# Performance work log

Measured on AMD Instinct MI355X. Metric: run time of the kernel, lower is better.

## Reference

```python
import jax, jax.numpy as jnp
import numpy as np

N_NODES = 50000


def _sage_mean(x, src, dst, Wl, bl, Wr, n_nodes):
    # PyG SAGEConv (aggr='mean', root_weight=True): lin_l(mean_j x_j) + lin_r(x_i)
    msgs = x[src]                                             # [E, F] gather
    agg = jax.ops.segment_sum(msgs, dst, num_segments=n_nodes)  # [N, F]
    cnt = jax.ops.segment_sum(jnp.ones((src.shape[0],), x.dtype), dst,
                              num_segments=n_nodes)           # [N]
    mean = agg / jnp.maximum(cnt, 1.0)[:, None]
    return mean @ Wl + bl + x @ Wr


def setup_inputs() -> dict:
    key = jax.random.key(0)
    ks = jax.random.split(key, 12)
    in_ft = 64
    o0, o1, o2 = 64, 128, 128
    d2 = o0 + o0          # conv2 in = 128
    d3 = o0 + o0 + o1     # conv3 in = 256
    E = 800000

    def lin(k, fi, fo):
        s = 1.0 / np.sqrt(fi)
        return jax.random.uniform(k, (fi, fo), jnp.float32, -s, s)

    x = jax.random.normal(ks[0], (N_NODES, in_ft), jnp.float32)
    edge_index = jax.random.randint(ks[1], (2, E), 0, N_NODES, jnp.int64)
    return {
        "x": x,
        "edge_index": edge_index,
        "Wp": lin(ks[2], in_ft, o0), "bp": jnp.zeros((o0,), jnp.float32),
        "Wl1": lin(ks[3], in_ft, o0), "bl1": jnp.zeros((o0,), jnp.float32),
        "Wr1": lin(ks[4], in_ft, o0),
        "Wl2": lin(ks[5], d2, o1), "bl2": jnp.zeros((o1,), jnp.float32),
        "Wr2": lin(ks[6], d2, o1),
        "Wl3": lin(ks[7], d3, o2), "bl3": jnp.zeros((o2,), jnp.float32),
        "Wr3": lin(ks[8], d3, o2),
    }


def reference(x, edge_index, Wp, bp, Wl1, bl1, Wr1, Wl2, bl2, Wr2, Wl3, bl3, Wr3):
    src, dst = edge_index[0], edge_index[1]
    act = jax.nn.relu
    x_p = act(x @ Wp + bp)                                        # [N, o0]
    h1 = act(_sage_mean(x, src, dst, Wl1, bl1, Wr1, N_NODES))      # [N, o0]
    in2 = jnp.concatenate([x_p, h1], axis=1)                      # [N, 2*o0]
    h2 = act(_sage_mean(in2, src, dst, Wl2, bl2, Wr2, N_NODES))    # [N, o1]
    in3 = jnp.concatenate([x_p, h1, h2], axis=1)                  # [N, 2*o0+o1]
    h3 = act(_sage_mean(in3, src, dst, Wl3, bl3, Wr3, N_NODES))    # [N, o2]
    return h3
```

## Files before the change

### kernel.cpp

```cpp
#include <hip/hip_runtime.h>

#define N_NODES 50000
#define ELLW 48

typedef unsigned int uint;
typedef unsigned short ushort;
typedef float floatx4 __attribute__((ext_vector_type(4)));
typedef short short8 __attribute__((ext_vector_type(8)));

__device__ inline ushort f2bf(float f) {
    uint u = __float_as_uint(f);
    return (ushort)((u + 0x7fffu + ((u >> 16) & 1u)) >> 16);
}
__device__ inline float bflo(uint u) { return __uint_as_float(u << 16); }
__device__ inline float bfhi(uint u) { return __uint_as_float(u & 0xffff0000u); }


__device__ inline void swz_body(const float* __restrict__ W, ushort* __restrict__ Wz,
                                int O, int t) {
    int lane = t & 63, cb = t >> 6;
    int NBm = O / 16;
    int c = cb / NBm, nb = cb % NBm;
    int quad = lane >> 4, l16 = lane & 15;
#pragma unroll
    for (int j = 0; j < 8; j++) {
        float v = W[(size_t)(c * 32 + quad * 8 + j) * O + nb * 16 + l16];
        Wz[(size_t)t * 8 + j] = f2bf(v);
    }
}

__device__ void gemm1_body(int gb, const float* __restrict__ x,
                           const float* __restrict__ Wp, const float* __restrict__ bp,
                           ushort* __restrict__ feats, ushort* ldsA) {
    constexpr int LDA = 40;
    const int tid = threadIdx.x;
    const int wave = tid >> 6, lane = tid & 63;
    const int quad = lane >> 4, l16 = lane & 15;
    const int node0 = gb * 64;

    floatx4 acc[4];
#pragma unroll
    for (int nb = 0; nb < 4; nb++) acc[nb] = (floatx4){0.f, 0.f, 0.f, 0.f};

#pragma unroll
    for (int kk = 0; kk < 2; kk++) {
        const int k0 = kk * 32;
        __syncthreads();
        {
            int row = tid >> 2, seg = tid & 3;
            int node = node0 + row;
            float4 v0 = {0.f,0.f,0.f,0.f}, v1 = {0.f,0.f,0.f,0.f};
            if (node < N_NODES) {
                v0 = *(const float4*)&x[(size_t)node * 64 + k0 + seg * 8];
                v1 = *(const float4*)&x[(size_t)node * 64 + k0 + seg * 8 + 4];
            }
            ushort4 o0, o1;
            o0.x = f2bf(v0.x); o0.y = f2bf(v0.y); o0.z = f2bf(v0.z); o0.w = f2bf(v0.w);
            o1.x = f2bf(v1.x); o1.y = f2bf(v1.y); o1.z = f2bf(v1.z); o1.w = f2bf(v1.w);
            *(ushort4*)&ldsA[row * LDA + seg * 8] = o0;
            *(ushort4*)&ldsA[row * LDA + seg * 8 + 4] = o1;
        }
        __syncthreads();

        short8 a = *(const short8*)&ldsA[(wave * 16 + l16) * LDA + quad * 8];
#pragma unroll
        for (int nb = 0; nb < 4; nb++) {
            short8 bfrag;
#pragma unroll
            for (int j = 0; j < 8; j++)
                bfrag[j] = (short)f2bf(Wp[(size_t)(k0 + quad * 8 + j) * 64 + nb * 16 + l16]);
            acc[nb] = __builtin_amdgcn_mfma_f32_16x16x32_bf16(a, bfrag, acc[nb], 0, 0, 0);
        }
    }

#pragma unroll
    for (int nb = 0; nb < 4; nb++) {
        int ncol = nb * 16 + l16;
        float bv = bp[ncol];
#pragma unroll
        for (int r = 0; r < 4; r++) {
            int node = node0 + wave * 16 + quad * 4 + r;
            if (node >= N_NODES) continue;
            float v = fmaxf(acc[nb][r] + bv, 0.f);
            feats[(size_t)node * 256 + ncol] = f2bf(v);
        }
    }
}

__global__ __launch_bounds__(256) void k1_mega(
    const int* __restrict__ src, const int* __restrict__ dst, int E,
    int* __restrict__ fillc, ushort* __restrict__ ell,
    const float* __restrict__ x, ushort* __restrict__ xb,
    const float* __restrict__ Wp, const float* __restrict__ bp, ushort* __restrict__ feats,
    const float* __restrict__ Wl1, ushort* __restrict__ zl1,
    const float* __restrict__ Wr1, ushort* __restrict__ zr1,
    const float* __restrict__ Wl2, ushort* __restrict__ zl2,
    const float* __restrict__ Wr2, ushort* __restrict__ zr2,
    const float* __restrict__ Wl3, ushort* __restrict__ zl3,
    const float* __restrict__ Wr3, ushort* __restrict__ zr3,
    int NF, int NG, int NC)
{
    __shared__ ushort ldsA[64 * 40];
    int b = blockIdx.x, tid = threadIdx.x;
    if (b < NF) {
        int t = b * 256 + tid;
        if (t < E) {
            int d = dst[t], s = src[t];
            int p = atomicAdd(&fillc[d], 1);
            if (p < ELLW) ell[(size_t)d * ELLW + p] = (ushort)s;
        }
        return;
    }
    b -= NF;
    if (b < NG) { gemm1_body(b, x, Wp, bp, feats, ldsA); return; }
    b -= NG;
    if (b < NC) {
        int t = b * 256 + tid;
        float4 v = ((const float4*)x)[t];
        ushort4 o;
        o.x = f2bf(v.x); o.y = f2bf(v.y); o.z = f2bf(v.z); o.w = f2bf(v.w);
        ((ushort4*)xb)[t] = o;
        return;
    }
    b -= NC;
    if      (b < 2)  swz_body(Wl1, zl1, 64,  (b - 0) * 256 + tid);
    else if (b < 4)  swz_body(Wr1, zr1, 64,  (b - 2) * 256 + tid);
    else if (b < 12) swz_body(Wl2, zl2, 128, (b - 4) * 256 + tid);
    else if (b < 20) swz_body(Wr2, zr2, 128, (b - 12) * 256 + tid);
    else if (b < 36) swz_body(Wl3, zl3, 128, (b - 20) * 256 + tid);
    else             swz_body(Wr3, zr3, 128, (b - 36) * 256 + tid);
}


__global__ __launch_bounds__(256) void gather64_k(const int* __restrict__ fillc,
                                                  const ushort* __restrict__ ell,
                                                  const ushort* __restrict__ in, int sin,
                                                  ushort* __restrict__ out, int sout) {
    int node = blockIdx.x * 4 + (threadIdx.x >> 6);
    if (node >= N_NODES) return;
    int lane = threadIdx.x & 63;
    int sub = lane >> 3, c = lane & 7;
    int n = fillc[node]; int nc = (n > ELLW) ? ELLW : n;
    const ushort* base = ell + (size_t)node * ELLW;
    float a[8];
#pragma unroll
    for (int j = 0; j < 8; j++) a[j] = 0.f;

    int i = sub;
    for (; i + 8 < nc; i += 16) {
        uint4 u0 = *(const uint4*)&in[(size_t)base[i] * sin + 8 * c];
        uint4 u1 = *(const uint4*)&in[(size_t)base[i + 8] * sin + 8 * c];
        a[0] += bflo(u0.x) + bflo(u1.x);  a[1] += bfhi(u0.x) + bfhi(u1.x);
        a[2] += bflo(u0.y) + bflo(u1.y);  a[3] += bfhi(u0.y) + bfhi(u1.y);
        a[4] += bflo(u0.z) + bflo(u1.z);  a[5] += bfhi(u0.z) + bfhi(u1.z);
        a[6] += bflo(u0.w) + bflo(u1.w);  a[7] += bfhi(u0.w) + bfhi(u1.w);
    }
    if (i < nc) {
        uint4 u0 = *(const uint4*)&in[(size_t)base[i] * sin + 8 * c];
        a[0] += bflo(u0.x);  a[1] += bfhi(u0.x);
        a[2] += bflo(u0.y);  a[3] += bfhi(u0.y);
        a[4] += bflo(u0.z);  a[5] += bfhi(u0.z);
        a[6] += bflo(u0.w);  a[7] += bfhi(u0.w);
    }
#pragma unroll
    for (int d = 8; d < 64; d <<= 1)
#pragma unroll
        for (int j = 0; j < 8; j++) a[j] += __shfl_xor(a[j], d);
    if (sub == 0) {
        float iv = 1.0f / fmaxf((float)n, 1.0f);
        uint4 r;
        r.x = (uint)f2bf(a[0] * iv) | ((uint)f2bf(a[1] * iv) << 16);
        r.y = (uint)f2bf(a[2] * iv) | ((uint)f2bf(a[3] * iv) << 16);
        r.z = (uint)f2bf(a[4] * iv) | ((uint)f2bf(a[5] * iv) << 16);
        r.w = (uint)f2bf(a[6] * iv) | ((uint)f2bf(a[7] * iv) << 16);
        *(uint4*)&out[(size_t)node * sout + 8 * c] = r;
    }
}

__global__ __launch_bounds__(256) void gather128_k(const int* __restrict__ fillc,
                                                   const ushort* __restrict__ ell,
                                                   const ushort* __restrict__ in, int sin,
                                                   ushort* __restrict__ out, int sout) {
    int node = blockIdx.x * 4 + (threadIdx.x >> 6);
    if (node >= N_NODES) return;
    int lane = threadIdx.x & 63;
    int sub = lane >> 4, c = lane & 15;
    int n = fillc[node]; int nc = (n > ELLW) ? ELLW : n;
    const ushort* base = ell + (size_t)node * ELLW;
    float a[8];
#pragma unroll
    for (int j = 0; j < 8; j++) a[j] = 0.f;

    int i = sub;
    for (; i + 12 < nc; i += 16) {
        uint4 u0 = *(const uint4*)&in[(size_t)base[i] * sin + 8 * c];
        uint4 u1 = *(const uint4*)&in[(size_t)base[i + 4] * sin + 8 * c];
        uint4 u2 = *(const uint4*)&in[(size_t)base[i + 8] * sin + 8 * c];
        uint4 u3 = *(const uint4*)&in[(size_t)base[i + 12] * sin + 8 * c];
        a[0] += (bflo(u0.x) + bflo(u1.x)) + (bflo(u2.x) + bflo(u3.x));
        a[1] += (bfhi(u0.x) + bfhi(u1.x)) + (bfhi(u2.x) + bfhi(u3.x));
        a[2] += (bflo(u0.y) + bflo(u1.y)) + (bflo(u2.y) + bflo(u3.y));
        a[3] += (bfhi(u0.y) + bfhi(u1.y)) + (bfhi(u2.y) + bfhi(u3.y));
        a[4] += (bflo(u0.z) + bflo(u1.z)) + (bflo(u2.z) + bflo(u3.z));
        a[5] += (bfhi(u0.z) + bfhi(u1.z)) + (bfhi(u2.z) + bfhi(u3.z));
        a[6] += (bflo(u0.w) + bflo(u1.w)) + (bflo(u2.w) + bflo(u3.w));
        a[7] += (bfhi(u0.w) + bfhi(u1.w)) + (bfhi(u2.w) + bfhi(u3.w));
    }
    for (; i < nc; i += 4) {
        uint4 u0 = *(const uint4*)&in[(size_t)base[i] * sin + 8 * c];
        a[0] += bflo(u0.x);  a[1] += bfhi(u0.x);
        a[2] += bflo(u0.y);  a[3] += bfhi(u0.y);
        a[4] += bflo(u0.z);  a[5] += bfhi(u0.z);
        a[6] += bflo(u0.w);  a[7] += bfhi(u0.w);
    }
#pragma unroll
    for (int d = 16; d < 64; d <<= 1)
#pragma unroll
        for (int j = 0; j < 8; j++) a[j] += __shfl_xor(a[j], d);
    if (sub == 0) {
        float iv = 1.0f / fmaxf((float)n, 1.0f);
        uint4 r;
        r.x = (uint)f2bf(a[0] * iv) | ((uint)f2bf(a[1] * iv) << 16);
        r.y = (uint)f2bf(a[2] * iv) | ((uint)f2bf(a[3] * iv) << 16);
        r.z = (uint)f2bf(a[4] * iv) | ((uint)f2bf(a[5] * iv) << 16);
        r.w = (uint)f2bf(a[6] * iv) | ((uint)f2bf(a[7] * iv) << 16);
        *(uint4*)&out[(size_t)node * sout + 8 * c] = r;
    }
}


template <int O, bool OUT_BF16>
__global__ __launch_bounds__(256) void mfma_gemm_k(
    const ushort* __restrict__ A1, int s1, int K1, const ushort* __restrict__ Wz1,
    const ushort* __restrict__ A2, int s2, int K2, const ushort* __restrict__ Wz2,
    const float* __restrict__ bias, void* __restrict__ outp, int so, int ocol)
{
    constexpr int NB = O / 16;
    constexpr int LDA = 40;
    __shared__ ushort ldsA[64 * LDA];

    const int tid = threadIdx.x;
    const int wave = tid >> 6, lane = tid & 63;
    const int quad = lane >> 4, l16 = lane & 15;
    const int node0 = blockIdx.x * 64;

    floatx4 acc[NB];
#pragma unroll
    for (int nb = 0; nb < NB; nb++) acc[nb] = (floatx4){0.f, 0.f, 0.f, 0.f};

#pragma unroll 1
    for (int phase = 0; phase < 2; ++phase) {
        const ushort* A = phase ? A2 : A1;
        const ushort* Wz = phase ? Wz2 : Wz1;
        const int K = phase ? K2 : K1;
        const int sA = phase ? s2 : s1;

#pragma unroll 1
        for (int k0 = 0; k0 < K; k0 += 32) {
            __syncthreads();
            {
                int row = tid >> 2, seg = tid & 3;
                int node = node0 + row;
                uint4 v = {0u, 0u, 0u, 0u};
                if (node < N_NODES)
                    v = *(const uint4*)&A[(size_t)node * sA + k0 + seg * 8];
                *(uint4*)&ldsA[row * LDA + seg * 8] = v;
            }
            __syncthreads();

            short8 a = *(const short8*)&ldsA[(wave * 16 + l16) * LDA + quad * 8];
            const short8* bz = (const short8*)Wz + (size_t)(k0 >> 5) * NB * 64;
#pragma unroll
            for (int nb = 0; nb < NB; nb++) {
                short8 b = bz[nb * 64 + lane];
                acc[nb] = __builtin_amdgcn_mfma_f32_16x16x32_bf16(a, b, acc[nb], 0, 0, 0);
            }
        }
    }

#pragma unroll
    for (int nb = 0; nb < NB; nb++) {
        int ncol = nb * 16 + l16;
        float bv = bias[ncol];
#pragma unroll
        for (int r = 0; r < 4; r++) {
            int node = node0 + wave * 16 + quad * 4 + r;
            if (node >= N_NODES) continue;
            float v = fmaxf(acc[nb][r] + bv, 0.f);
            if (OUT_BF16)
                ((ushort*)outp)[(size_t)node * so + ocol + ncol] = f2bf(v);
            else
                ((float*)outp)[(size_t)node * so + ocol + ncol] = v;
        }
    }
}


extern "C" void kernel_launch(void* const* d_in, const int* in_sizes, int n_in,
                              void* d_out, int out_size, void* d_ws, size_t ws_size,
                              hipStream_t stream) {
    const float* x   = (const float*)d_in[0];
    const int*   ei  = (const int*)d_in[1];
    const float* Wp  = (const float*)d_in[2];
    const float* bp  = (const float*)d_in[3];
    const float* Wl1 = (const float*)d_in[4];
    const float* bl1 = (const float*)d_in[5];
    const float* Wr1 = (const float*)d_in[6];
    const float* Wl2 = (const float*)d_in[7];
    const float* bl2 = (const float*)d_in[8];
    const float* Wr2 = (const float*)d_in[9];
    const float* Wl3 = (const float*)d_in[10];
    const float* bl3 = (const float*)d_in[11];
    const float* Wr3 = (const float*)d_in[12];

    const int E = in_sizes[1] / 2;
    const int N = N_NODES;
    const int* src = ei;
    const int* dst = ei + E;

    char* p = (char*)d_ws;
    ushort* xb    = (ushort*)p;  p += (size_t)N * 64 * 2;
    ushort* feats = (ushort*)p;  p += (size_t)N * 256 * 2;
    ushort* aggx  = (ushort*)p;  p += (size_t)N * 64 * 2;
    ushort* aggf  = (ushort*)p;  p += (size_t)N * 256 * 2;
    int* fillc    = (int*)p;     p += (size_t)N * 4;
    ushort* ell   = (ushort*)p;  p += (size_t)N * ELLW * 2;
    ushort* zl1   = (ushort*)p;  p += 64 * 64 * 2;
    ushort* zr1   = (ushort*)p;  p += 64 * 64 * 2;
    ushort* zl2   = (ushort*)p;  p += 128 * 128 * 2;
    ushort* zr2   = (ushort*)p;  p += 128 * 128 * 2;
    ushort* zl3   = (ushort*)p;  p += 256 * 128 * 2;
    ushort* zr3   = (ushort*)p;  p += 256 * 128 * 2;

    hipMemsetAsync(fillc, 0, (size_t)N * sizeof(int), stream);

    const int NF = (E + 255) / 256;
    const int NG = (N + 63) / 64;
    const int NC = (N * 64 / 4) / 256;

    k1_mega<<<NF + NG + NC + 52, 256, 0, stream>>>(
        src, dst, E, fillc, ell, x, xb, Wp, bp, feats,
        Wl1, zl1, Wr1, zr1, Wl2, zl2, Wr2, zr2, Wl3, zl3, Wr3, zr3,
        NF, NG, NC);

    gather64_k<<<(N + 3) / 4, 256, 0, stream>>>(fillc, ell, xb, 64, aggx, 64);

    mfma_gemm_k<64, true><<<NG, 256, 0, stream>>>(
        aggx, 64, 64, zl1, xb, 64, 64, zr1, bl1, feats, 256, 64);

    gather128_k<<<(N + 3) / 4, 256, 0, stream>>>(fillc, ell, feats, 256, aggf, 256);

    mfma_gemm_k<128, true><<<NG, 256, 0, stream>>>(
        aggf, 256, 128, zl2, feats, 256, 128, zr2, bl2, feats, 256, 128);

    gather128_k<<<(N + 3) / 4, 256, 0, stream>>>(fillc, ell, feats + 128, 256, aggf + 128, 256);

    mfma_gemm_k<128, false><<<NG, 256, 0, stream>>>(
        aggf, 256, 256, zl3, feats, 256, 256, zr3, bl3, (float*)d_out, 128, 0);
}
```

Measured before the change: 291.4 us.

## Project layer-1 features before aggregation and fuse x_p gather with it

```diff
diff --git a/kernel.cpp b/kernel.cpp
--- a/kernel.cpp
+++ b/kernel.cpp
@@ -14,7 +14,9 @@
 }
 __device__ inline float bflo(uint u) { return __uint_as_float(u << 16); }
 __device__ inline float bfhi(uint u) { return __uint_as_float(u & 0xffff0000u); }
-
+__device__ inline uint pack2(float lo, float hi) {
+    return (uint)f2bf(lo) | ((uint)f2bf(hi) << 16);
+}
 
 __device__ inline void swz_body(const float* __restrict__ W, ushort* __restrict__ Wz,
                                 int O, int t) {
@@ -31,16 +33,22 @@
 
 __device__ void gemm1_body(int gb, const float* __restrict__ x,
                            const float* __restrict__ Wp, const float* __restrict__ bp,
-                           ushort* __restrict__ feats, ushort* ldsA) {
+                           const float* __restrict__ Wl1, const float* __restrict__ Wr1,
+                           ushort* __restrict__ feats, ushort* __restrict__ g1in,
+                           ushort* __restrict__ r1, ushort* ldsA) {
     constexpr int LDA = 40;
     const int tid = threadIdx.x;
     const int wave = tid >> 6, lane = tid & 63;
     const int quad = lane >> 4, l16 = lane & 15;
     const int node0 = gb * 64;
 
-    floatx4 acc[4];
-#pragma unroll
-    for (int nb = 0; nb < 4; nb++) acc[nb] = (floatx4){0.f, 0.f, 0.f, 0.f};
+    floatx4 aP[4], aY[4], aR[4];
+#pragma unroll
+    for (int nb = 0; nb < 4; nb++) {
+        aP[nb] = (floatx4){0, 0, 0, 0};
+        aY[nb] = (floatx4){0, 0, 0, 0};
+        aR[nb] = (floatx4){0, 0, 0, 0};
+    }
 
 #pragma unroll
     for (int kk = 0; kk < 2; kk++) {
@@ -49,7 +57,7 @@
         {
             int row = tid >> 2, seg = tid & 3;
             int node = node0 + row;
-            float4 v0 = {0.f,0.f,0.f,0.f}, v1 = {0.f,0.f,0.f,0.f};
+            float4 v0 = {0, 0, 0, 0}, v1 = {0, 0, 0, 0};
             if (node < N_NODES) {
                 v0 = *(const float4*)&x[(size_t)node * 64 + k0 + seg * 8];
                 v1 = *(const float4*)&x[(size_t)node * 64 + k0 + seg * 8 + 4];
@@ -65,11 +73,19 @@
         short8 a = *(const short8*)&ldsA[(wave * 16 + l16) * LDA + quad * 8];
 #pragma unroll
         for (int nb = 0; nb < 4; nb++) {
-            short8 bfrag;
+            short8 bw;
 #pragma unroll
             for (int j = 0; j < 8; j++)
-                bfrag[j] = (short)f2bf(Wp[(size_t)(k0 + quad * 8 + j) * 64 + nb * 16 + l16]);
-            acc[nb] = __builtin_amdgcn_mfma_f32_16x16x32_bf16(a, bfrag, acc[nb], 0, 0, 0);
+                bw[j] = (short)f2bf(Wp[(size_t)(k0 + quad * 8 + j) * 64 + nb * 16 + l16]);
+            aP[nb] = __builtin_amdgcn_mfma_f32_16x16x32_bf16(a, bw, aP[nb], 0, 0, 0);
+#pragma unroll
+            for (int j = 0; j < 8; j++)
+                bw[j] = (short)f2bf(Wl1[(size_t)(k0 + quad * 8 + j) * 64 + nb * 16 + l16]);
+            aY[nb] = __builtin_amdgcn_mfma_f32_16x16x32_bf16(a, bw, aY[nb], 0, 0, 0);
+#pragma unroll
+            for (int j = 0; j < 8; j++)
+                bw[j] = (short)f2bf(Wr1[(size_t)(k0 + quad * 8 + j) * 64 + nb * 16 + l16]);
+            aR[nb] = __builtin_amdgcn_mfma_f32_16x16x32_bf16(a, bw, aR[nb], 0, 0, 0);
         }
     }
 
@@ -81,8 +97,11 @@
         for (int r = 0; r < 4; r++) {
             int node = node0 + wave * 16 + quad * 4 + r;
             if (node >= N_NODES) continue;
-            float v = fmaxf(acc[nb][r] + bv, 0.f);
-            feats[(size_t)node * 256 + ncol] = f2bf(v);
+            ushort xp = f2bf(fmaxf(aP[nb][r] + bv, 0.f));
+            feats[(size_t)node * 256 + ncol] = xp;
+            g1in[(size_t)node * 128 + 64 + ncol] = xp;
+            g1in[(size_t)node * 128 + ncol] = f2bf(aY[nb][r]);
+            r1[(size_t)node * 64 + ncol] = f2bf(aR[nb][r]);
         }
     }
 }
@@ -90,15 +109,15 @@
 __global__ __launch_bounds__(256) void k1_mega(
     const int* __restrict__ src, const int* __restrict__ dst, int E,
     int* __restrict__ fillc, ushort* __restrict__ ell,
-    const float* __restrict__ x, ushort* __restrict__ xb,
-    const float* __restrict__ Wp, const float* __restrict__ bp, ushort* __restrict__ feats,
-    const float* __restrict__ Wl1, ushort* __restrict__ zl1,
-    const float* __restrict__ Wr1, ushort* __restrict__ zr1,
+    const float* __restrict__ x,
+    const float* __restrict__ Wp, const float* __restrict__ bp,
+    const float* __restrict__ Wl1, const float* __restrict__ Wr1,
+    ushort* __restrict__ feats, ushort* __restrict__ g1in, ushort* __restrict__ r1,
     const float* __restrict__ Wl2, ushort* __restrict__ zl2,
     const float* __restrict__ Wr2, ushort* __restrict__ zr2,
     const float* __restrict__ Wl3, ushort* __restrict__ zl3,
     const float* __restrict__ Wr3, ushort* __restrict__ zr3,
-    int NF, int NG, int NC)
+    int NF, int NG)
 {
     __shared__ ushort ldsA[64 * 40];
     int b = blockIdx.x, tid = threadIdx.x;
@@ -112,75 +131,20 @@
         return;
     }
     b -= NF;
-    if (b < NG) { gemm1_body(b, x, Wp, bp, feats, ldsA); return; }
+    if (b < NG) { gemm1_body(b, x, Wp, bp, Wl1, Wr1, feats, g1in, r1, ldsA); return; }
     b -= NG;
-    if (b < NC) {
-        int t = b * 256 + tid;
-        float4 v = ((const float4*)x)[t];
-        ushort4 o;
-        o.x = f2bf(v.x); o.y = f2bf(v.y); o.z = f2bf(v.z); o.w = f2bf(v.w);
-        ((ushort4*)xb)[t] = o;
-        return;
-    }
-    b -= NC;
-    if      (b < 2)  swz_body(Wl1, zl1, 64,  (b - 0) * 256 + tid);
-    else if (b < 4)  swz_body(Wr1, zr1, 64,  (b - 2) * 256 + tid);
-    else if (b < 12) swz_body(Wl2, zl2, 128, (b - 4) * 256 + tid);
-    else if (b < 20) swz_body(Wr2, zr2, 128, (b - 12) * 256 + tid);
-    else if (b < 36) swz_body(Wl3, zl3, 128, (b - 20) * 256 + tid);
-    else             swz_body(Wr3, zr3, 128, (b - 36) * 256 + tid);
-}
-
-
-__global__ __launch_bounds__(256) void gather64_k(const int* __restrict__ fillc,
-                                                  const ushort* __restrict__ ell,
-                                                  const ushort* __restrict__ in, int sin,
-                                                  ushort* __restrict__ out, int sout) {
-    int node = blockIdx.x * 4 + (threadIdx.x >> 6);
-    if (node >= N_NODES) return;
-    int lane = threadIdx.x & 63;
-    int sub = lane >> 3, c = lane & 7;
-    int n = fillc[node]; int nc = (n > ELLW) ? ELLW : n;
-    const ushort* base = ell + (size_t)node * ELLW;
-    float a[8];
-#pragma unroll
-    for (int j = 0; j < 8; j++) a[j] = 0.f;
-
-    int i = sub;
-    for (; i + 8 < nc; i += 16) {
-        uint4 u0 = *(const uint4*)&in[(size_t)base[i] * sin + 8 * c];
-        uint4 u1 = *(const uint4*)&in[(size_t)base[i + 8] * sin + 8 * c];
-        a[0] += bflo(u0.x) + bflo(u1.x);  a[1] += bfhi(u0.x) + bfhi(u1.x);
-        a[2] += bflo(u0.y) + bflo(u1.y);  a[3] += bfhi(u0.y) + bfhi(u1.y);
-        a[4] += bflo(u0.z) + bflo(u1.z);  a[5] += bfhi(u0.z) + bfhi(u1.z);
-        a[6] += bflo(u0.w) + bflo(u1.w);  a[7] += bfhi(u0.w) + bfhi(u1.w);
-    }
-    if (i < nc) {
-        uint4 u0 = *(const uint4*)&in[(size_t)base[i] * sin + 8 * c];
-        a[0] += bflo(u0.x);  a[1] += bfhi(u0.x);
-        a[2] += bflo(u0.y);  a[3] += bfhi(u0.y);
-        a[4] += bflo(u0.z);  a[5] += bfhi(u0.z);
-        a[6] += bflo(u0.w);  a[7] += bfhi(u0.w);
-    }
-#pragma unroll
-    for (int d = 8; d < 64; d <<= 1)
-#pragma unroll
-        for (int j = 0; j < 8; j++) a[j] += __shfl_xor(a[j], d);
-    if (sub == 0) {
-        float iv = 1.0f / fmaxf((float)n, 1.0f);
-        uint4 r;
-        r.x = (uint)f2bf(a[0] * iv) | ((uint)f2bf(a[1] * iv) << 16);
-        r.y = (uint)f2bf(a[2] * iv) | ((uint)f2bf(a[3] * iv) << 16);
-        r.z = (uint)f2bf(a[4] * iv) | ((uint)f2bf(a[5] * iv) << 16);
-        r.w = (uint)f2bf(a[6] * iv) | ((uint)f2bf(a[7] * iv) << 16);
-        *(uint4*)&out[(size_t)node * sout + 8 * c] = r;
-    }
-}
-
-__global__ __launch_bounds__(256) void gather128_k(const int* __restrict__ fillc,
-                                                   const ushort* __restrict__ ell,
-                                                   const ushort* __restrict__ in, int sin,
-                                                   ushort* __restrict__ out, int sout) {
+    if      (b < 8)  swz_body(Wl2, zl2, 128, (b - 0) * 256 + tid);
+    else if (b < 16) swz_body(Wr2, zr2, 128, (b - 8) * 256 + tid);
+    else if (b < 32) swz_body(Wl3, zl3, 128, (b - 16) * 256 + tid);
+    else             swz_body(Wr3, zr3, 128, (b - 32) * 256 + tid);
+}
+
+
+__global__ __launch_bounds__(256) void gather_split_k(const int* __restrict__ fillc,
+                                                      const ushort* __restrict__ ell,
+                                                      const ushort* __restrict__ in, int sin,
+                                                      ushort* __restrict__ dA, int sA,
+                                                      ushort* __restrict__ dB, int sB) {
     int node = blockIdx.x * 4 + (threadIdx.x >> 6);
     if (node >= N_NODES) return;
     int lane = threadIdx.x & 63;
@@ -214,20 +178,99 @@
         a[6] += bflo(u0.w);  a[7] += bfhi(u0.w);
     }
 #pragma unroll
-    for (int d = 16; d < 64; d <<= 1)
-#pragma unroll
-        for (int j = 0; j < 8; j++) a[j] += __shfl_xor(a[j], d);
+    for (int j = 0; j < 8; j++) {
+        a[j] += __shfl_xor(a[j], 16);
+        a[j] += __shfl_xor(a[j], 32);
+    }
     if (sub == 0) {
         float iv = 1.0f / fmaxf((float)n, 1.0f);
         uint4 r;
-        r.x = (uint)f2bf(a[0] * iv) | ((uint)f2bf(a[1] * iv) << 16);
-        r.y = (uint)f2bf(a[2] * iv) | ((uint)f2bf(a[3] * iv) << 16);
-        r.z = (uint)f2bf(a[4] * iv) | ((uint)f2bf(a[5] * iv) << 16);
-        r.w = (uint)f2bf(a[6] * iv) | ((uint)f2bf(a[7] * iv) << 16);
+        r.x = pack2(a[0] * iv, a[1] * iv);
+        r.y = pack2(a[2] * iv, a[3] * iv);
+        r.z = pack2(a[4] * iv, a[5] * iv);
+        r.w = pack2(a[6] * iv, a[7] * iv);
+        if (c < 8) *(uint4*)&dA[(size_t)node * sA + 8 * c] = r;
+        else       *(uint4*)&dB[(size_t)node * sB + 8 * (c - 8)] = r;
+    }
+}
+
+__global__ __launch_bounds__(256) void gather64_k(const int* __restrict__ fillc,
+                                                  const ushort* __restrict__ ell,
+                                                  const ushort* __restrict__ in, int sin,
+                                                  ushort* __restrict__ out, int sout) {
+    int wid = blockIdx.x * 4 + (threadIdx.x >> 6);
+    int lane = threadIdx.x & 63;
+    int half = lane >> 5;
+    int node = wid * 2 + half;
+    if (node >= N_NODES) return;
+    int l32 = lane & 31;
+    int sub = l32 >> 3, c = l32 & 7;
+    int n = fillc[node]; int nc = (n > ELLW) ? ELLW : n;
+    const ushort* base = ell + (size_t)node * ELLW;
+    float a[8];
+#pragma unroll
+    for (int j = 0; j < 8; j++) a[j] = 0.f;
+
+    int i = sub;
+    for (; i + 12 < nc; i += 16) {
+        uint4 u0 = *(const uint4*)&in[(size_t)base[i] * sin + 8 * c];
+        uint4 u1 = *(const uint4*)&in[(size_t)base[i + 4] * sin + 8 * c];
+        uint4 u2 = *(const uint4*)&in[(size_t)base[i + 8] * sin + 8 * c];
+        uint4 u3 = *(const uint4*)&in[(size_t)base[i + 12] * sin + 8 * c];
+        a[0] += (bflo(u0.x) + bflo(u1.x)) + (bflo(u2.x) + bflo(u3.x));
+        a[1] += (bfhi(u0.x) + bfhi(u1.x)) + (bfhi(u2.x) + bfhi(u3.x));
+        a[2] += (bflo(u0.y) + bflo(u1.y)) + (bflo(u2.y) + bflo(u3.y));
+        a[3] += (bfhi(u0.y) + bfhi(u1.y)) + (bfhi(u2.y) + bfhi(u3.y));
+        a[4] += (bflo(u0.z) + bflo(u1.z)) + (bflo(u2.z) + bflo(u3.z));
+        a[5] += (bfhi(u0.z) + bfhi(u1.z)) + (bfhi(u2.z) + bfhi(u3.z));
+        a[6] += (bflo(u0.w) + bflo(u1.w)) + (bflo(u2.w) + bflo(u3.w));
+        a[7] += (bfhi(u0.w) + bfhi(u1.w)) + (bfhi(u2.w) + bfhi(u3.w));
+    }
+    for (; i < nc; i += 4) {
+        uint4 u0 = *(const uint4*)&in[(size_t)base[i] * sin + 8 * c];
+        a[0] += bflo(u0.x);  a[1] += bfhi(u0.x);
+        a[2] += bflo(u0.y);  a[3] += bfhi(u0.y);
+        a[4] += bflo(u0.z);  a[5] += bfhi(u0.z);
+        a[6] += bflo(u0.w);  a[7] += bfhi(u0.w);
+    }
+#pragma unroll
+    for (int j = 0; j < 8; j++) {
+        a[j] += __shfl_xor(a[j], 8);
+        a[j] += __shfl_xor(a[j], 16);
+    }
+    if (sub == 0) {
+        float iv = 1.0f / fmaxf((float)n, 1.0f);
+        uint4 r;
+        r.x = pack2(a[0] * iv, a[1] * iv);
+        r.y = pack2(a[2] * iv, a[3] * iv);
+        r.z = pack2(a[4] * iv, a[5] * iv);
+        r.w = pack2(a[6] * iv, a[7] * iv);
         *(uint4*)&out[(size_t)node * sout + 8 * c] = r;
     }
 }
 
+__global__ __launch_bounds__(256) void h1ew_k(const ushort* __restrict__ aggY1,
+                                              const ushort* __restrict__ r1,
+                                              const float* __restrict__ bl1,
+                                              ushort* __restrict__ feats) {
+    int t = blockIdx.x * 256 + threadIdx.x;
+    if (t >= N_NODES * 8) return;
+    int node = t >> 3, c0 = (t & 7) * 8;
+    uint4 a = *(const uint4*)&aggY1[(size_t)node * 64 + c0];
+    uint4 b = *(const uint4*)&r1[(size_t)node * 64 + c0];
+    float4 b0 = *(const float4*)&bl1[c0];
+    float4 b1 = *(const float4*)&bl1[c0 + 4];
+    uint4 o;
+    o.x = pack2(fmaxf(bflo(a.x) + bflo(b.x) + b0.x, 0.f),
+                fmaxf(bfhi(a.x) + bfhi(b.x) + b0.y, 0.f));
+    o.y = pack2(fmaxf(bflo(a.y) + bflo(b.y) + b0.z, 0.f),
+                fmaxf(bfhi(a.y) + bfhi(b.y) + b0.w, 0.f));
+    o.z = pack2(fmaxf(bflo(a.z) + bflo(b.z) + b1.x, 0.f),
+                fmaxf(bfhi(a.z) + bfhi(b.z) + b1.y, 0.f));
+    o.w = pack2(fmaxf(bflo(a.w) + bflo(b.w) + b1.z, 0.f),
+                fmaxf(bfhi(a.w) + bfhi(b.w) + b1.w, 0.f));
+    *(uint4*)&feats[(size_t)node * 256 + 64 + c0] = o;
+}
 
 template <int O, bool OUT_BF16>
 __global__ __launch_bounds__(256) void mfma_gemm_k(
@@ -246,7 +289,7 @@
 
     floatx4 acc[NB];
 #pragma unroll
-    for (int nb = 0; nb < NB; nb++) acc[nb] = (floatx4){0.f, 0.f, 0.f, 0.f};
+    for (int nb = 0; nb < NB; nb++) acc[nb] = (floatx4){0, 0, 0, 0};
 
 #pragma unroll 1
     for (int phase = 0; phase < 2; ++phase) {
@@ -261,7 +304,7 @@
             {
                 int row = tid >> 2, seg = tid & 3;
                 int node = node0 + row;
-                uint4 v = {0u, 0u, 0u, 0u};
+                uint4 v = {0, 0, 0, 0};
                 if (node < N_NODES)
                     v = *(const uint4*)&A[(size_t)node * sA + k0 + seg * 8];
                 *(uint4*)&ldsA[row * LDA + seg * 8] = v;
@@ -319,14 +362,13 @@
     const int* dst = ei + E;
 
     char* p = (char*)d_ws;
-    ushort* xb    = (ushort*)p;  p += (size_t)N * 64 * 2;
     ushort* feats = (ushort*)p;  p += (size_t)N * 256 * 2;
-    ushort* aggx  = (ushort*)p;  p += (size_t)N * 64 * 2;
+    ushort* g1in  = (ushort*)p;  p += (size_t)N * 128 * 2;
+    ushort* aggY1 = (ushort*)p;  p += (size_t)N * 64 * 2;
     ushort* aggf  = (ushort*)p;  p += (size_t)N * 256 * 2;
+    ushort* r1    = (ushort*)p;  p += (size_t)N * 64 * 2;
     int* fillc    = (int*)p;     p += (size_t)N * 4;
     ushort* ell   = (ushort*)p;  p += (size_t)N * ELLW * 2;
-    ushort* zl1   = (ushort*)p;  p += 64 * 64 * 2;
-    ushort* zr1   = (ushort*)p;  p += 64 * 64 * 2;
     ushort* zl2   = (ushort*)p;  p += 128 * 128 * 2;
     ushort* zr2   = (ushort*)p;  p += 128 * 128 * 2;
     ushort* zl3   = (ushort*)p;  p += 256 * 128 * 2;
@@ -336,24 +378,23 @@
 
     const int NF = (E + 255) / 256;
     const int NG = (N + 63) / 64;
-    const int NC = (N * 64 / 4) / 256;
-
-    k1_mega<<<NF + NG + NC + 52, 256, 0, stream>>>(
-        src, dst, E, fillc, ell, x, xb, Wp, bp, feats,
-        Wl1, zl1, Wr1, zr1, Wl2, zl2, Wr2, zr2, Wl3, zl3, Wr3, zr3,
-        NF, NG, NC);
-
-    gather64_k<<<(N + 3) / 4, 256, 0, stream>>>(fillc, ell, xb, 64, aggx, 64);
-
-    mfma_gemm_k<64, true><<<NG, 256, 0, stream>>>(
-        aggx, 64, 64, zl1, xb, 64, 64, zr1, bl1, feats, 256, 64);
-
-    gather128_k<<<(N + 3) / 4, 256, 0, stream>>>(fillc, ell, feats, 256, aggf, 256);
+
+    k1_mega<<<NF + NG + 48, 256, 0, stream>>>(
+        src, dst, E, fillc, ell, x, Wp, bp, Wl1, Wr1, feats, g1in, r1,
+        Wl2, zl2, Wr2, zr2, Wl3, zl3, Wr3, zr3, NF, NG);
+
+    gather_split_k<<<(N + 3) / 4, 256, 0, stream>>>(
+        fillc, ell, g1in, 128, aggY1, 64, aggf, 256);
+
+    h1ew_k<<<(N * 8 + 255) / 256, 256, 0, stream>>>(aggY1, r1, bl1, feats);
+
+    gather64_k<<<(N + 7) / 8, 256, 0, stream>>>(fillc, ell, feats + 64, 256, aggf + 64, 256);
 
     mfma_gemm_k<128, true><<<NG, 256, 0, stream>>>(
         aggf, 256, 128, zl2, feats, 256, 128, zr2, bl2, feats, 256, 128);
 
-    gather128_k<<<(N + 3) / 4, 256, 0, stream>>>(fillc, ell, feats + 128, 256, aggf + 128, 256);
+    gather_split_k<<<(N + 3) / 4, 256, 0, stream>>>(
+        fillc, ell, feats + 128, 256, aggf + 128, 256, aggf + 192, 256);
 
     mfma_gemm_k<128, false><<<NG, 256, 0, stream>>>(
         aggf, 256, 256, zl3, feats, 256, 256, zr3, bl3, (float*)d_out, 128, 0);
```

Result: no change. 295.6 us (+1.4%).
